# Performance work log

Measured on AMD Instinct MI355X. Metric: run time of the kernel, lower is better.

## Reference

```python
import jax, jax.numpy as jnp
import numpy as np

NHEAD = 8
HEAD_DIM = 32
AREA_WIDTH = 4
H = 32   # coarse grid height (hw0_c == hw1_c, agg_scale already applied)
W = 40   # coarse grid width
C_MAX = max(H, W) * AREA_WIDTH  # max_candidate_num = 160


def _skew(t):
    # t: [N,3] -> [N,3,3] cross-product matrix
    z = jnp.zeros_like(t[:, 0])
    return jnp.stack([
        jnp.stack([z, -t[:, 2], t[:, 1]], -1),
        jnp.stack([t[:, 2], z, -t[:, 0]], -1),
        jnp.stack([-t[:, 1], t[:, 0], z], -1),
    ], -2)


def _candidate_info(K0, K1, R, t):
    # Pixel coords in (x, y) order, as kornia.create_meshgrid(..., normalized=False)
    ys, xs = jnp.meshgrid(jnp.arange(H, dtype=jnp.float32),
                          jnp.arange(W, dtype=jnp.float32), indexing='ij')
    coord = jnp.stack([xs, ys], -1).reshape(-1, 2)  # [S,2]
    S = coord.shape[0]
    # Fundamental matrix F = K1^{-T} [t]_x R K0^{-1}
    F = jnp.swapaxes(jnp.linalg.inv(K1), -1, -2) @ _skew(t) @ R @ jnp.linalg.inv(K0)
    p = jnp.concatenate([coord, jnp.ones((S, 1), jnp.float32)], -1)  # [S,3] homogeneous
    lines = jnp.einsum('nij,lj->nli', F, p)  # [N,L,3] epipolar lines a*u+b*v+c=0 in image1
    a, b, c = lines[..., 0], lines[..., 1], lines[..., 2]
    mode = jnp.abs(b) > jnp.abs(a)  # True: parametrize v = f(u); False: u = f(v)
    b_safe = jnp.where(mode, b, 1.0)
    a_safe = jnp.where(mode, 1.0, a)
    # v(u) band check
    coord_y = (-a / b_safe)[..., None] * coord[:, 0] + (-c / b_safe)[..., None]  # [N,L,S]
    within_y = (coord[:, 1] < coord_y + AREA_WIDTH / 2.0) & (coord[:, 1] > coord_y - AREA_WIDTH / 2.0)
    # u(v) band check
    coord_x = (-b / a_safe)[..., None] * coord[:, 1] + (-c / a_safe)[..., None]  # [N,L,S]
    within_x = (coord[:, 0] < coord_x + AREA_WIDTH / 2.0) & (coord[:, 0] > coord_x - AREA_WIDTH / 2.0)
    within = jnp.where(mode[..., None], within_y, within_x)  # [N,L,S]
    # gather_index: keep the C_MAX largest source indices whose mask bit is set
    idx = jnp.arange(S)
    true_idx = jnp.where(within, idx, 0)           # [N,L,S]
    true_idx = jnp.sort(true_idx, axis=-1)
    c_index = true_idx[..., -C_MAX:]               # [N,L,C]
    valid = c_index != 0                           # index 0 treated as invalid (as in original)
    return c_index, valid


def setup_inputs() -> dict:
    key = jax.random.key(0)
    kq, kk, kv = jax.random.split(key, 3)
    N = 1
    feat = NHEAD * HEAD_DIM
    query = jax.random.normal(kq, (N, H, W, feat), jnp.float32)
    key_t = jax.random.normal(kk, (N, H, W, feat), jnp.float32)
    value = jax.random.normal(kv, (N, H, W, feat), jnp.float32)
    f = 35.0
    Kmat = jnp.array([[[f, 0.0, W / 2.0], [0.0, f, H / 2.0], [0.0, 0.0, 1.0]]], jnp.float32)
    R = jnp.eye(3, dtype=jnp.float32)[None]
    t = jnp.array([[1.0, 0.15, 0.02]], jnp.float32)
    return {"query": query, "key": key_t, "value": value, "K0": Kmat, "K1": Kmat, "R": R, "t": t}


def reference(query, key, value, K0, K1, R, t):
    c_index, valid = _candidate_info(K0, K1, R, t)  # [N,L,C] int / bool (no-grad constants)
    N = query.shape[0]
    L = H * W
    q = query.reshape(N, L, NHEAD, HEAD_DIM)
    k = key.reshape(N, L, NHEAD, HEAD_DIM)
    v = value.reshape(N, L, NHEAD, HEAD_DIM)
    n_idx = jnp.arange(N)[:, None, None]
    k_g = k[n_idx, c_index]  # [N,L,C,nhead,d]
    v_g = v[n_idx, c_index]  # [N,L,C,nhead,d]
    qk = jnp.einsum('nlhd,nlchd->nlch', q, k_g)
    scale = 1.0 / jnp.sqrt(jnp.float32(HEAD_DIM))
    scores = jnp.where(valid[..., None], qk * scale, -jnp.inf)
    A = jnp.nan_to_num(jax.nn.softmax(scores, axis=2), nan=0.0)  # fully-masked rows -> 0
    return jnp.einsum('nlch,nlchd->nlhd', A, v_g)  # [N,L,nhead,d]
```

## Files before the change

### kernel.cpp

```cpp
#include <hip/hip_runtime.h>
#include <math.h>

#define NHEAD 8
#define HEAD_DIM 32
#define IMG_H 32
#define IMG_W 40
#define NPIX (IMG_H*IMG_W)
#define CMAX 160
#define NITER (CMAX/8)
#define FEAT (NHEAD*HEAD_DIM)


__device__ __forceinline__ void np_inv3x3_reg(const float* __restrict__ M, float inv[3][3]) {
#pragma clang fp contract(off)
    float a00=M[0], a01=M[1], a02=M[2];
    float a10=M[3], a11=M[4], a12=M[5];
    float a20=M[6], a21=M[7], a22=M[8];

    const float c0 = fabsf(a00), c1 = fabsf(a10), c2 = fabsf(a20);
    const bool s1 = c1 > c0;
    const float cm = s1 ? c1 : c0;
    const bool s2 = c2 > cm;
    const bool q1 = s1 && !s2;
    const bool q2 = s2;
    {
        const float n0 = q2 ? a20 : (q1 ? a10 : a00);
        const float n1 = q2 ? a21 : (q1 ? a11 : a01);
        const float n2 = q2 ? a22 : (q1 ? a12 : a02);
        const float m0 = q1 ? a00 : a10, m1 = q1 ? a01 : a11, m2 = q1 ? a02 : a12;
        const float r0 = q2 ? a00 : a20, r1 = q2 ? a01 : a21, r2 = q2 ? a02 : a22;
        a00=n0; a01=n1; a02=n2;
        a10=m0; a11=m1; a12=m2;
        a20=r0; a21=r1; a22=r2;
    }
    const float rp0 = 1.0f / a00;
    a10 = a10 * rp0;
    a20 = a20 * rp0;
    a11 = a11 - a10*a01;
    a12 = a12 - a10*a02;
    a21 = a21 - a20*a01;
    a22 = a22 - a20*a02;

    const bool sB = fabsf(a21) > fabsf(a11);
    {
        const float t0 = sB ? a20 : a10, t1 = sB ? a21 : a11, t2 = sB ? a22 : a12;
        const float u0 = sB ? a10 : a20, u1 = sB ? a11 : a21, u2 = sB ? a12 : a22;
        a10=t0; a11=t1; a12=t2;
        a20=u0; a21=u1; a22=u2;
    }
    const float rp1 = 1.0f / a11;
    a21 = a21 * rp1;
    a22 = a22 - a21*a12;

    #pragma unroll
    for (int col = 0; col < 3; col++) {
        float b0 = (col==0) ? 1.0f : 0.0f;
        float b1 = (col==1) ? 1.0f : 0.0f;
        float b2 = (col==2) ? 1.0f : 0.0f;
        {
            const float w0 = q2 ? b2 : (q1 ? b1 : b0);
            const float w1 = q1 ? b0 : b1;
            const float w2 = q2 ? b0 : b2;
            b0=w0; b1=w1; b2=w2;
        }
        {
            const float x1 = sB ? b2 : b1;
            const float x2 = sB ? b1 : b2;
            b1=x1; b2=x2;
        }
        b1 = b1 - a10*b0;
        b2 = b2 - a20*b0;
        b2 = b2 - a21*b1;
        b2 = b2 / a22;
        b0 = b0 - a02*b2;
        b1 = b1 - a12*b2;
        b1 = b1 / a11;
        b0 = b0 - a01*b1;
        b0 = b0 / a00;
        inv[0][col]=b0; inv[1][col]=b1; inv[2][col]=b2;
    }
}

__device__ __forceinline__ void mm3_chain(const float A[3][3], const float B[3][3], float C[3][3]) {
#pragma clang fp contract(off)
    for (int i=0;i<3;i++)
        for (int j=0;j<3;j++) {
            float acc = A[i][0]*B[0][j];
            acc = acc + A[i][1]*B[1][j];
            acc = acc + A[i][2]*B[2][j];
            C[i][j] = acc;
        }
}
__device__ __forceinline__ void mm3_fma(const float A[3][3], const float B[3][3], float C[3][3]) {
#pragma clang fp contract(off)
    for (int i=0;i<3;i++)
        for (int j=0;j<3;j++) {
            float acc = A[i][0]*B[0][j];
            acc = __builtin_fmaf(A[i][1], B[1][j], acc);
            acc = __builtin_fmaf(A[i][2], B[2][j], acc);
            C[i][j] = acc;
        }
}
__device__ __forceinline__ float einsum_row(const float Fi[3], float x, float y) {
#pragma clang fp contract(off)
    float acc = Fi[0]*x;
    acc = acc + Fi[1]*y;
    acc = acc + Fi[2]*1.0f;
    return acc;
}


__global__ __launch_bounds__(512) void one2many_fused(
    const float* __restrict__ q, const float* __restrict__ k, const float* __restrict__ v,
    const float* __restrict__ K0, const float* __restrict__ K1,
    const float* __restrict__ R, const float* __restrict__ t,
    float* __restrict__ out)
{
#pragma clang fp contract(off)
    __shared__ int s_cand[CMAX];
    __shared__ int s_cnt;

    const int bx  = blockIdx.x;
    const int l   = (bx >> 3) + (bx & 7) * 160;
    const int tid = threadIdx.x;

    if (tid == 0) s_cnt = 0;

    const int h    = tid >> 6;
    const int lane = tid & 63;
    const int grp  = lane >> 3;
    const int dj   = (lane & 7) << 2;

    const float4 q4 = *(const float4*)(q + l*FEAT + h*HEAD_DIM + dj);

    float slope, icpt; bool mode;
    {
        float i0[3][3], i1[3][3], A[3][3], B[3][3], T1[3][3], T2[3][3], Fm[3][3], Rm[3][3];
        np_inv3x3_reg(K0, i0);
        np_inv3x3_reg(K1, i1);
        for (int i=0;i<3;i++)
            for (int j=0;j<3;j++) { A[i][j] = i1[j][i]; Rm[i][j] = R[i*3+j]; }
        const float t0=t[0], t1=t[1], t2=t[2];
        B[0][0]=0.f;  B[0][1]=-t2;  B[0][2]=t1;
        B[1][0]=t2;   B[1][1]=0.f;  B[1][2]=-t0;
        B[2][0]=-t1;  B[2][1]=t0;   B[2][2]=0.f;
        mm3_chain(A,B,T1);
        mm3_chain(T1,Rm,T2);
        mm3_fma(T2,i0,Fm);
        const float xl = (float)(l % IMG_W);
        const float yl = (float)(l / IMG_W);
        const float la = einsum_row(Fm[0], xl, yl);
        const float lb = einsum_row(Fm[1], xl, yl);
        const float lc = einsum_row(Fm[2], xl, yl);
        mode = fabsf(lb) > fabsf(la);
        const float denom = mode ? lb : la;
        slope = (mode ? -la : -lb) / denom;
        icpt  = (-lc) / denom;
    }

    __syncthreads();

    for (int m = tid; m < NPIX; m += 512) {
        const float xm = (float)(m % IMG_W), ym = (float)(m / IMG_W);
        const float tin  = mode ? xm : ym;
        const float tchk = mode ? ym : xm;
        const float mu = slope * tin;
        const float cc = mu + icpt;
        const float hi = cc + 2.0f;
        const float lo = cc - 2.0f;
        if ((tchk < hi) && (tchk > lo) && m != 0) {
            int pos = atomicAdd(&s_cnt, 1);
            if (pos < CMAX) s_cand[pos] = m;
        }
    }
    __syncthreads();
    const int nc = min(s_cnt, CMAX);

    const float* kh = k + h*HEAD_DIM + dj;
    const float* vh = v + h*HEAD_DIM + dj;

    float ax = 0.f, ay = 0.f, az = 0.f, aw = 0.f, ps = 0.f;
    #pragma unroll
    for (int i = 0; i < NITER; i++) {
        const int ci  = (i << 3) + grp;
        const int row = s_cand[(ci < nc) ? ci : 0];
        const size_t off = (size_t)row * FEAT;
        const float4 kk = *(const float4*)(kh + off);
        const float4 vv = *(const float4*)(vh + off);
        float p = q4.x*kk.x;
        p = __builtin_fmaf(q4.y, kk.y, p);
        p = __builtin_fmaf(q4.z, kk.z, p);
        p = __builtin_fmaf(q4.w, kk.w, p);
        p += __shfl_xor(p, 1);
        p += __shfl_xor(p, 2);
        p += __shfl_xor(p, 4);
        const float e = (ci < nc) ? __expf(p * 0.17677669529663687f) : 0.0f;
        ps += e;
        ax = __builtin_fmaf(e, vv.x, ax);
        ay = __builtin_fmaf(e, vv.y, ay);
        az = __builtin_fmaf(e, vv.z, az);
        aw = __builtin_fmaf(e, vv.w, aw);
    }

    #pragma unroll
    for (int o = 8; o <= 32; o <<= 1) {
        ax += __shfl_xor(ax, o);
        ay += __shfl_xor(ay, o);
        az += __shfl_xor(az, o);
        aw += __shfl_xor(aw, o);
        ps += __shfl_xor(ps, o);
    }

    if (lane < 8) {
        float4 r;
        if (nc > 0) { r.x = ax/ps; r.y = ay/ps; r.z = az/ps; r.w = aw/ps; }
        else        { r.x = r.y = r.z = r.w = 0.0f; }
        *(float4*)(out + l*FEAT + h*HEAD_DIM + dj) = r;
    }
}

extern "C" void kernel_launch(void* const* d_in, const int* in_sizes, int n_in,
                              void* d_out, int out_size, void* d_ws, size_t ws_size,
                              hipStream_t stream) {
    const float* q  = (const float*)d_in[0];
    const float* k  = (const float*)d_in[1];
    const float* v  = (const float*)d_in[2];
    const float* K0 = (const float*)d_in[3];
    const float* K1 = (const float*)d_in[4];
    const float* R  = (const float*)d_in[5];
    const float* t  = (const float*)d_in[6];
    float* out = (float*)d_out;
    (void)d_ws; (void)ws_size;
    one2many_fused<<<NPIX, 512, 0, stream>>>(q, k, v, K0, K1, R, t, out);
}
```

Before: 87.91 us.

## Process four heads per wavefront with 128-thread blocks

Shrinks each block from 8 wavefronts (one head each) to 2 wavefronts that each handle 4 heads, launching 128 threads per block. Per-block work that is repeated (the F-matrix setup, the candidate scan, the shared-memory index reads) is now spread over fewer threads, and each wavefront issues more independent loads per iteration. The cost is more registers per thread and less per-block parallelism.

```diff
diff --git a/kernel.cpp b/kernel.cpp
--- a/kernel.cpp
+++ b/kernel.cpp
@@ -110,7 +110,7 @@
 }
 
 
-__global__ __launch_bounds__(512) void one2many_fused(
+__global__ __launch_bounds__(128, 4) void one2many_fused(
     const float* __restrict__ q, const float* __restrict__ k, const float* __restrict__ v,
     const float* __restrict__ K0, const float* __restrict__ K1,
     const float* __restrict__ R, const float* __restrict__ t,
@@ -126,12 +126,16 @@
 
     if (tid == 0) s_cnt = 0;
 
-    const int h    = tid >> 6;
+    const int w    = tid >> 6;
+    const int hb   = w << 2;
     const int lane = tid & 63;
     const int grp  = lane >> 3;
     const int dj   = (lane & 7) << 2;
 
-    const float4 q4 = *(const float4*)(q + l*FEAT + h*HEAD_DIM + dj);
+    float4 q4[4];
+    #pragma unroll
+    for (int j = 0; j < 4; j++)
+        q4[j] = *(const float4*)(q + l*FEAT + (hb+j)*HEAD_DIM + dj);
 
     float slope, icpt; bool mode;
     {
@@ -160,7 +164,7 @@
 
     __syncthreads();
 
-    for (int m = tid; m < NPIX; m += 512) {
+    for (int m = tid; m < NPIX; m += 128) {
         const float xm = (float)(m % IMG_W), ym = (float)(m / IMG_W);
         const float tin  = mode ? xm : ym;
         const float tchk = mode ? ym : xm;
@@ -176,46 +180,65 @@
     __syncthreads();
     const int nc = min(s_cnt, CMAX);
 
-    const float* kh = k + h*HEAD_DIM + dj;
-    const float* vh = v + h*HEAD_DIM + dj;
-
-    float ax = 0.f, ay = 0.f, az = 0.f, aw = 0.f, ps = 0.f;
+    const float* kbase = k + hb*HEAD_DIM + dj;
+    const float* vbase = v + hb*HEAD_DIM + dj;
+
+    float ax[4], ay[4], az[4], aw[4], ps[4];
+    #pragma unroll
+    for (int j = 0; j < 4; j++) { ax[j]=0.f; ay[j]=0.f; az[j]=0.f; aw[j]=0.f; ps[j]=0.f; }
+
     #pragma unroll
     for (int i = 0; i < NITER; i++) {
         const int ci  = (i << 3) + grp;
         const int row = s_cand[(ci < nc) ? ci : 0];
         const size_t off = (size_t)row * FEAT;
-        const float4 kk = *(const float4*)(kh + off);
-        const float4 vv = *(const float4*)(vh + off);
-        float p = q4.x*kk.x;
-        p = __builtin_fmaf(q4.y, kk.y, p);
-        p = __builtin_fmaf(q4.z, kk.z, p);
-        p = __builtin_fmaf(q4.w, kk.w, p);
-        p += __shfl_xor(p, 1);
-        p += __shfl_xor(p, 2);
-        p += __shfl_xor(p, 4);
-        const float e = (ci < nc) ? __expf(p * 0.17677669529663687f) : 0.0f;
-        ps += e;
-        ax = __builtin_fmaf(e, vv.x, ax);
-        ay = __builtin_fmaf(e, vv.y, ay);
-        az = __builtin_fmaf(e, vv.z, az);
-        aw = __builtin_fmaf(e, vv.w, aw);
+        const bool live = (ci < nc);
+
+        float4 k4[4], v4[4];
+        #pragma unroll
+        for (int j = 0; j < 4; j++) {
+            k4[j] = *(const float4*)(kbase + off + j*HEAD_DIM);
+            v4[j] = *(const float4*)(vbase + off + j*HEAD_DIM);
+        }
+
+        #pragma unroll
+        for (int j = 0; j < 4; j++) {
+            float p = q4[j].x*k4[j].x;
+            p = __builtin_fmaf(q4[j].y, k4[j].y, p);
+            p = __builtin_fmaf(q4[j].z, k4[j].z, p);
+            p = __builtin_fmaf(q4[j].w, k4[j].w, p);
+            p += __shfl_xor(p, 1);
+            p += __shfl_xor(p, 2);
+            p += __shfl_xor(p, 4);
+            const float e = live ? __expf(p * 0.17677669529663687f) : 0.0f;
+            ps[j] += e;
+            ax[j] = __builtin_fmaf(e, v4[j].x, ax[j]);
+            ay[j] = __builtin_fmaf(e, v4[j].y, ay[j]);
+            az[j] = __builtin_fmaf(e, v4[j].z, az[j]);
+            aw[j] = __builtin_fmaf(e, v4[j].w, aw[j]);
+        }
     }
 
     #pragma unroll
     for (int o = 8; o <= 32; o <<= 1) {
-        ax += __shfl_xor(ax, o);
-        ay += __shfl_xor(ay, o);
-        az += __shfl_xor(az, o);
-        aw += __shfl_xor(aw, o);
-        ps += __shfl_xor(ps, o);
+        #pragma unroll
+        for (int j = 0; j < 4; j++) {
+            ax[j] += __shfl_xor(ax[j], o);
+            ay[j] += __shfl_xor(ay[j], o);
+            az[j] += __shfl_xor(az[j], o);
+            aw[j] += __shfl_xor(aw[j], o);
+            ps[j] += __shfl_xor(ps[j], o);
+        }
     }
 
     if (lane < 8) {
-        float4 r;
-        if (nc > 0) { r.x = ax/ps; r.y = ay/ps; r.z = az/ps; r.w = aw/ps; }
-        else        { r.x = r.y = r.z = r.w = 0.0f; }
-        *(float4*)(out + l*FEAT + h*HEAD_DIM + dj) = r;
+        #pragma unroll
+        for (int j = 0; j < 4; j++) {
+            float4 r;
+            if (nc > 0) { r.x = ax[j]/ps[j]; r.y = ay[j]/ps[j]; r.z = az[j]/ps[j]; r.w = aw[j]/ps[j]; }
+            else        { r.x = r.y = r.z = r.w = 0.0f; }
+            *(float4*)(out + l*FEAT + (hb+j)*HEAD_DIM + dj) = r;
+        }
     }
 }
 
@@ -231,5 +254,5 @@
     const float* t  = (const float*)d_in[6];
     float* out = (float*)d_out;
     (void)d_ws; (void)ws_size;
-    one2many_fused<<<NPIX, 512, 0, stream>>>(q, k, v, K0, K1, R, t, out);
-}
+    one2many_fused<<<NPIX, 128, 0, stream>>>(q, k, v, K0, K1, R, t, out);
+}
```

Result: slower. 102.7 us (+16.8%).

## Remap work so each wave covers all heads over a quarter of candidates

Applied to the files above, without the earlier changes.

The block shrinks from 512 to 256 threads, and the thread-to-work mapping changes. Each 64-lane wave now covers the full 256-wide feature row (all 8 heads) for a contiguous quarter of the candidate list, using a wave-uniform candidate index via readfirstlane. Each gather is therefore one contiguous 1KB row per wave instead of scattered 128-byte head slices across 8 candidates. Partial sums from the four waves are combined through shared memory with a block barrier, which adds LDS traffic and one more sync in exchange for better-coalesced K/V loads and fewer threads per block.

```diff
diff --git a/kernel.cpp b/kernel.cpp
--- a/kernel.cpp
+++ b/kernel.cpp
@@ -7,7 +7,7 @@
 #define IMG_W 40
 #define NPIX (IMG_H*IMG_W)
 #define CMAX 160
-#define NITER (CMAX/8)
+#define CPW (CMAX/4)
 #define FEAT (NHEAD*HEAD_DIM)
 
 
@@ -110,7 +110,7 @@
 }
 
 
-__global__ __launch_bounds__(512) void one2many_fused(
+__global__ __launch_bounds__(256) void one2many_fused(
     const float* __restrict__ q, const float* __restrict__ k, const float* __restrict__ v,
     const float* __restrict__ K0, const float* __restrict__ K1,
     const float* __restrict__ R, const float* __restrict__ t,
@@ -119,6 +119,7 @@
 #pragma clang fp contract(off)
     __shared__ int s_cand[CMAX];
     __shared__ int s_cnt;
+    __shared__ float s_ax[256], s_ay[256], s_az[256], s_aw[256], s_ps[256];
 
     const int bx  = blockIdx.x;
     const int l   = (bx >> 3) + (bx & 7) * 160;
@@ -126,12 +127,10 @@
 
     if (tid == 0) s_cnt = 0;
 
-    const int h    = tid >> 6;
+    const int w    = tid >> 6;
     const int lane = tid & 63;
-    const int grp  = lane >> 3;
-    const int dj   = (lane & 7) << 2;
-
-    const float4 q4 = *(const float4*)(q + l*FEAT + h*HEAD_DIM + dj);
+
+    const float4 q4 = *(const float4*)(q + l*FEAT + (lane << 2));
 
     float slope, icpt; bool mode;
     {
@@ -160,7 +159,7 @@
 
     __syncthreads();
 
-    for (int m = tid; m < NPIX; m += 512) {
+    for (int m = tid; m < NPIX; m += 256) {
         const float xm = (float)(m % IMG_W), ym = (float)(m / IMG_W);
         const float tin  = mode ? xm : ym;
         const float tchk = mode ? ym : xm;
@@ -176,17 +175,19 @@
     __syncthreads();
     const int nc = min(s_cnt, CMAX);
 
-    const float* kh = k + h*HEAD_DIM + dj;
-    const float* vh = v + h*HEAD_DIM + dj;
+    const float* kl = k + (lane << 2);
+    const float* vl = v + (lane << 2);
 
     float ax = 0.f, ay = 0.f, az = 0.f, aw = 0.f, ps = 0.f;
+    const int cbase = w * CPW;
     #pragma unroll
-    for (int i = 0; i < NITER; i++) {
-        const int ci  = (i << 3) + grp;
-        const int row = s_cand[(ci < nc) ? ci : 0];
+    for (int i = 0; i < CPW; i++) {
+        const int ci   = cbase + i;
+        const bool live = (ci < nc);
+        const int row  = __builtin_amdgcn_readfirstlane(s_cand[live ? ci : 0]);
         const size_t off = (size_t)row * FEAT;
-        const float4 kk = *(const float4*)(kh + off);
-        const float4 vv = *(const float4*)(vh + off);
+        const float4 kk = *(const float4*)(kl + off);
+        const float4 vv = *(const float4*)(vl + off);
         float p = q4.x*kk.x;
         p = __builtin_fmaf(q4.y, kk.y, p);
         p = __builtin_fmaf(q4.z, kk.z, p);
@@ -194,7 +195,7 @@
         p += __shfl_xor(p, 1);
         p += __shfl_xor(p, 2);
         p += __shfl_xor(p, 4);
-        const float e = (ci < nc) ? __expf(p * 0.17677669529663687f) : 0.0f;
+        const float e = live ? __expf(p * 0.17677669529663687f) : 0.0f;
         ps += e;
         ax = __builtin_fmaf(e, vv.x, ax);
         ay = __builtin_fmaf(e, vv.y, ay);
@@ -202,20 +203,19 @@
         aw = __builtin_fmaf(e, vv.w, aw);
     }
 
-    #pragma unroll
-    for (int o = 8; o <= 32; o <<= 1) {
-        ax += __shfl_xor(ax, o);
-        ay += __shfl_xor(ay, o);
-        az += __shfl_xor(az, o);
-        aw += __shfl_xor(aw, o);
-        ps += __shfl_xor(ps, o);
-    }
-
-    if (lane < 8) {
+    s_ax[tid] = ax; s_ay[tid] = ay; s_az[tid] = az; s_aw[tid] = aw; s_ps[tid] = ps;
+    __syncthreads();
+
+    if (tid < 64) {
+        const float fax = ((s_ax[tid] + s_ax[tid+64]) + s_ax[tid+128]) + s_ax[tid+192];
+        const float fay = ((s_ay[tid] + s_ay[tid+64]) + s_ay[tid+128]) + s_ay[tid+192];
+        const float faz = ((s_az[tid] + s_az[tid+64]) + s_az[tid+128]) + s_az[tid+192];
+        const float faw = ((s_aw[tid] + s_aw[tid+64]) + s_aw[tid+128]) + s_aw[tid+192];
+        const float fps = ((s_ps[tid] + s_ps[tid+64]) + s_ps[tid+128]) + s_ps[tid+192];
         float4 r;
-        if (nc > 0) { r.x = ax/ps; r.y = ay/ps; r.z = az/ps; r.w = aw/ps; }
+        if (nc > 0) { r.x = fax/fps; r.y = fay/fps; r.z = faz/fps; r.w = faw/fps; }
         else        { r.x = r.y = r.z = r.w = 0.0f; }
-        *(float4*)(out + l*FEAT + h*HEAD_DIM + dj) = r;
+        *(float4*)(out + l*FEAT + (tid << 2)) = r;
     }
 }
 
@@ -231,5 +231,5 @@
     const float* t  = (const float*)d_in[6];
     float* out = (float*)d_out;
     (void)d_ws; (void)ws_size;
-    one2many_fused<<<NPIX, 512, 0, stream>>>(q, k, v, K0, K1, R, t, out);
-}
+    one2many_fused<<<NPIX, 256, 0, stream>>>(q, k, v, K0, K1, R, t, out);
+}
```

Measured after the change: 83.37 us. 5.2% less time.
